# Kernel tuning notes

Hardware: AMD Instinct MI355X
Metric: run time of the kernel (lower is better)

## Reference

```python
import jax, jax.numpy as jnp
import numpy as np

TEMP = 0.5  # init kwarg `tmp`
NUM_CLASSES = 100


def setup_inputs() -> dict:
    key = jax.random.key(0)
    k1, k2 = jax.random.split(key)
    embedding = jax.random.normal(k1, (8192, 256), dtype=jnp.float32)
    label = jax.random.randint(k2, (8192,), 0, NUM_CLASSES, dtype=jnp.int64)
    return {"embedding": embedding, "label": label}


def reference(embedding, label):
    # Row-normalize -> pairwise cosine similarity [N, N]
    normed = embedding / jnp.linalg.norm(embedding, axis=1, keepdims=True)
    sim = (normed @ normed.T) / TEMP  # already divided by temperature

    N = embedding.shape[0]
    eye = jnp.eye(N, dtype=bool)

    # Denominator: sum of exp(sim) over off-diagonal entries per row
    exp_sim = jnp.exp(sim)
    row_sum = jnp.sum(jnp.where(eye, 0.0, exp_sim), axis=1)  # [N]

    # log(exp(sim_ij) / row_sum_i) = sim_ij - log(row_sum_i)
    log_prob = sim - jnp.log(row_sum)[:, None]

    # Positive mask: same label, i != j
    pos_mask = (label[:, None] == label[None, :]) & ~eye
    n_i = jnp.sum(pos_mask, axis=1)  # positives per anchor

    inner = jnp.sum(jnp.where(pos_mask, log_prob, 0.0), axis=1)  # [N]
    per_anchor = jnp.where(n_i > 0, -inner / jnp.maximum(n_i, 1).astype(sim.dtype), 0.0)
    return jnp.sum(per_anchor)
```

## Files before the change

kernel.cpp:

```cpp
#include <hip/hip_runtime.h>
#include <hip/hip_bf16.h>
#include <stdint.h>

#define N    8192
#define D    256
#define NCLS 100

static constexpr float TEMP    = 0.5f;
static constexpr float SCALE_F = 1.69864360f;
static constexpr float LN2     = 0.69314718055994531f;

typedef float f32x4 __attribute__((ext_vector_type(4)));

__device__ __forceinline__ unsigned short f2bf(float f) {
  union { float f; unsigned int u; } x; x.f = f;
  unsigned int r = x.u + 0x7fffu + ((x.u >> 16) & 1u);
  return (unsigned short)(r >> 16);
}
__device__ __forceinline__ float bf2f(unsigned short b) {
  union { unsigned int u; float f; } x; x.u = ((unsigned int)b) << 16;
  return x.f;
}


__global__ __launch_bounds__(256) void normalize_kernel(
    const float* __restrict__ emb, const long long* __restrict__ label,
    unsigned short* __restrict__ abf, unsigned char* __restrict__ a8,
    float* __restrict__ rowsum, int* __restrict__ cnt,
    int* __restrict__ list) {
  const int row  = blockIdx.x * 4 + (threadIdx.x >> 6);
  const int lane = threadIdx.x & 63;
  const float4 v = ((const float4*)(emb + (size_t)row * D))[lane];
  float ss = v.x * v.x + v.y * v.y + v.z * v.z + v.w * v.w;
#pragma unroll
  for (int off = 1; off < 64; off <<= 1) ss += __shfl_xor(ss, off);
  const float s = rsqrtf(ss) * SCALE_F;
  const float x = v.x * s, y = v.y * s, z = v.z * s, wv = v.w * s;

  ushort4 o;
  o.x = f2bf(x); o.y = f2bf(y); o.z = f2bf(z); o.w = f2bf(wv);
  ((ushort4*)(abf + (size_t)row * D))[lane] = o;

  int p = __builtin_amdgcn_cvt_pk_fp8_f32(x, y, 0, false);
  p = __builtin_amdgcn_cvt_pk_fp8_f32(z, wv, p, true);
  *(int*)(a8 + (size_t)(row >> 4) * 4096 + (lane >> 1) * 128 +
          (row & 15) * 8 + (lane & 1) * 4) = p;

  if (lane == 0) {
    rowsum[row] = 0.f;
    const int c = (int)label[row];
    const int slot = atomicAdd(cnt + c, 1);
    list[c * 256 + slot] = row;
  }
}

__global__ __launch_bounds__(256, 4) void simexp_rowsum_kernel(
    const unsigned char* __restrict__ A, float* __restrict__ rowsum) {
  const int tid  = threadIdx.x;
  const int w    = tid >> 6;
  const int lane = tid & 63;
  const int quad = lane >> 4;
  const int l15  = lane & 15;

  const int b = blockIdx.x;
  int x = (int)((-1.0f + sqrtf(1.0f + 8.0f * (float)b)) * 0.5f);
  while ((x + 1) * (x + 2) / 2 <= b) ++x;
  while (x * (x + 1) / 2 > b) --x;
  const int y = b - x * (x + 1) / 2;

  const int row0 = y << 7;
  const int col0 = x << 7;
  const bool diag = (x == y);
  const int wm  = (w & 1) * 64;
  const int jn0 = (w >> 1) * 64;
  if (diag && wm > jn0) return;
  const bool needmask = diag && (wm == jn0);

  const unsigned char* Ap = A + (size_t)((row0 >> 4) + (w & 1) * 4) * 4096;
  const unsigned char* Bp = A + (size_t)((col0 >> 4) + (w >> 1) * 4) * 4096;

  f32x4 acc[4][4];
#pragma unroll
  for (int mt = 0; mt < 4; ++mt)
#pragma unroll
    for (int nt = 0; nt < 4; ++nt) acc[mt][nt] = (f32x4){0.f, 0.f, 0.f, 0.f};

#pragma unroll
  for (int kq = 0; kq < 4; ++kq) {
#pragma unroll
    for (int kkl = 0; kkl < 2; ++kkl) {
      const int fo = kq * 1024 + (kkl * 4 + quad) * 128 + l15 * 8;
      long af[4], bf[4];
#pragma unroll
      for (int mt = 0; mt < 4; ++mt)
        af[mt] = *(const long*)(Ap + mt * 4096 + fo);
#pragma unroll
      for (int nt = 0; nt < 4; ++nt)
        bf[nt] = *(const long*)(Bp + nt * 4096 + fo);
#pragma unroll
      for (int mt = 0; mt < 4; ++mt)
#pragma unroll
        for (int nt = 0; nt < 4; ++nt)
          acc[mt][nt] = __builtin_amdgcn_mfma_f32_16x16x32_fp8_fp8(
              af[mt], bf[nt], acc[mt][nt], 0, 0, 0);
    }
  }

  float rowpart[4][4];
  float colpart[4] = {0.f, 0.f, 0.f, 0.f};
#pragma unroll
  for (int mt = 0; mt < 4; ++mt)
#pragma unroll
    for (int e = 0; e < 4; ++e) rowpart[mt][e] = 0.f;
#pragma unroll
  for (int mt = 0; mt < 4; ++mt)
#pragma unroll
    for (int nt = 0; nt < 4; ++nt)
#pragma unroll
      for (int e = 0; e < 4; ++e) {
        float v = __builtin_amdgcn_exp2f(acc[mt][nt][e]);
        if (needmask) {
          const int iw = mt * 16 + quad * 4 + e;
          const int jw = nt * 16 + l15;
          v = (iw < jw) ? v : 0.f;
        }
        rowpart[mt][e] += v;
        colpart[nt] += v;
      }

#pragma unroll
  for (int nt = 0; nt < 4; ++nt) {
    float v = colpart[nt];
    v += __shfl_xor(v, 16);
    v += __shfl_xor(v, 32);
    if (quad == 0)
      atomicAdd(&rowsum[col0 + jn0 + nt * 16 + l15], v);
  }
#pragma unroll
  for (int mt = 0; mt < 4; ++mt)
#pragma unroll
    for (int e = 0; e < 4; ++e) {
      float v = rowpart[mt][e];
      v += __shfl_xor(v, 1);
      v += __shfl_xor(v, 2);
      v += __shfl_xor(v, 4);
      v += __shfl_xor(v, 8);
      if (l15 == 0)
        atomicAdd(&rowsum[row0 + wm + mt * 16 + quad * 4 + e], v);
    }
}

__global__ __launch_bounds__(256) void finalize_kernel(
    const unsigned short* __restrict__ abf, const float* __restrict__ rowsum,
    const long long* __restrict__ label, const int* __restrict__ cnt,
    const int* __restrict__ list, float* __restrict__ out) {
  __shared__ float red[4];
  __shared__ int rows_l[256];
  const int tid  = threadIdx.x;
  const int w    = tid >> 6;
  const int lane = tid & 63;

  if (blockIdx.x < NCLS) {
    const int c = blockIdx.x;
    const int m = cnt[c];
    if (m <= 1) return;
    if (tid < m) rows_l[tid] = list[c * 256 + tid];
    __syncthreads();
    float acc = 0.f;
    for (int s = 0; s < m; ++s)
      acc += bf2f(abf[(size_t)rows_l[s] * D + tid]);
    float v = acc * acc;
#pragma unroll
    for (int off = 1; off < 64; off <<= 1) v += __shfl_xor(v, off);
    if (lane == 0) red[w] = v;
    __syncthreads();
    if (tid == 0) {
      const float ssq = red[0] + red[1] + red[2] + red[3];
      const float term = (ssq * LN2 - 2.0f * (float)m) / (float)(m - 1);
      atomicAdd(out, -term);
    }
  } else {
    const int i = (blockIdx.x - NCLS) * 256 + tid;
    const int c = (int)label[i];
    float v = 0.f;
    if (cnt[c] > 1)
      v = __builtin_amdgcn_logf(rowsum[i]) * LN2;
#pragma unroll
    for (int off = 1; off < 64; off <<= 1) v += __shfl_xor(v, off);
    if (lane == 0) red[w] = v;
    __syncthreads();
    if (tid == 0)
      atomicAdd(out, red[0] + red[1] + red[2] + red[3]);
  }
}

extern "C" void kernel_launch(void* const* d_in, const int* in_sizes, int n_in,
                              void* d_out, int out_size, void* d_ws,
                              size_t ws_size, hipStream_t stream) {
  const float* emb = (const float*)d_in[0];
  const long long* label = (const long long*)d_in[1];
  float* out = (float*)d_out;

  char* ws = (char*)d_ws;
  unsigned short* abf = (unsigned short*)ws;
  unsigned char* a8 = (unsigned char*)(ws + (size_t)N * D * 2);
  float* rowsum = (float*)(ws + (size_t)N * D * 3);
  int* cnt = (int*)(rowsum + N);
  int* list = cnt + 128;

  hipMemsetAsync(cnt, 0, 128 * 4, stream);
  hipMemsetAsync(out, 0, sizeof(float), stream);

  normalize_kernel<<<N / 4, 256, 0, stream>>>(emb, label, abf, a8, rowsum,
                                              cnt, list);

  simexp_rowsum_kernel<<<2080, 256, 0, stream>>>(a8, rowsum);

  finalize_kernel<<<NCLS + N / 256, 256, 0, stream>>>(abf, rowsum, label, cnt,
                                                      list, out);
}
```

Measured before the change: 135.9 us.

## Replace rowsum atomics with deterministic partial-sum slots reduced in finalize

Each wave of the triangular similarity kernel now writes its row and column partial exp-sums to dedicated slots in a per-band partial buffer instead of doing global atomicAdds on rowsum. The finalize kernel sums the 130 slots for each row before taking the log. Skipped diagonal waves zero their slots so every slot is written. This removes atomic contention and the rowsum zeroing, at the cost of a larger workspace and a strided 130-element reduction per row in finalize.

```diff
diff --git a/kernel.cpp b/kernel.cpp
--- a/kernel.cpp
+++ b/kernel.cpp
@@ -9,6 +9,8 @@
 static constexpr float TEMP    = 0.5f;
 static constexpr float SCALE_F = 1.69864360f;
 static constexpr float LN2     = 0.69314718055994531f;
+
+#define NSLOT 130
 
 typedef float f32x4 __attribute__((ext_vector_type(4)));
 
@@ -26,8 +28,7 @@
 __global__ __launch_bounds__(256) void normalize_kernel(
     const float* __restrict__ emb, const long long* __restrict__ label,
     unsigned short* __restrict__ abf, unsigned char* __restrict__ a8,
-    float* __restrict__ rowsum, int* __restrict__ cnt,
-    int* __restrict__ list) {
+    int* __restrict__ cnt, int* __restrict__ list) {
   const int row  = blockIdx.x * 4 + (threadIdx.x >> 6);
   const int lane = threadIdx.x & 63;
   const float4 v = ((const float4*)(emb + (size_t)row * D))[lane];
@@ -47,7 +48,6 @@
           (row & 15) * 8 + (lane & 1) * 4) = p;
 
   if (lane == 0) {
-    rowsum[row] = 0.f;
     const int c = (int)label[row];
     const int slot = atomicAdd(cnt + c, 1);
     list[c * 256 + slot] = row;
@@ -55,7 +55,7 @@
 }
 
 __global__ __launch_bounds__(256, 4) void simexp_rowsum_kernel(
-    const unsigned char* __restrict__ A, float* __restrict__ rowsum) {
+    const unsigned char* __restrict__ A, float* __restrict__ part) {
   const int tid  = threadIdx.x;
   const int w    = tid >> 6;
   const int lane = tid & 63;
@@ -73,7 +73,12 @@
   const bool diag = (x == y);
   const int wm  = (w & 1) * 64;
   const int jn0 = (w >> 1) * 64;
-  if (diag && wm > jn0) return;
+
+  if (diag && wm > jn0) {
+    part[((size_t)y * NSLOT + 2 * x + 0) * 128 + 64 + lane] = 0.f;
+    part[((size_t)x * NSLOT + 128 + 1) * 128 + lane] = 0.f;
+    return;
+  }
   const bool needmask = diag && (wm == jn0);
 
   const unsigned char* Ap = A + (size_t)((row0 >> 4) + (w & 1) * 4) * 4096;
@@ -128,13 +133,17 @@
         colpart[nt] += v;
       }
 
+  const int rslot = 2 * x + (jn0 >> 6);
+  const int cslot = diag ? (128 + (wm >> 6)) : (2 * y + (wm >> 6));
+  float* rowdst = part + ((size_t)y * NSLOT + rslot) * 128 + wm;
+  float* coldst = part + ((size_t)x * NSLOT + cslot) * 128 + jn0;
+
 #pragma unroll
   for (int nt = 0; nt < 4; ++nt) {
     float v = colpart[nt];
     v += __shfl_xor(v, 16);
     v += __shfl_xor(v, 32);
-    if (quad == 0)
-      atomicAdd(&rowsum[col0 + jn0 + nt * 16 + l15], v);
+    if (quad == 0) coldst[nt * 16 + l15] = v;
   }
 #pragma unroll
   for (int mt = 0; mt < 4; ++mt)
@@ -145,13 +154,12 @@
       v += __shfl_xor(v, 2);
       v += __shfl_xor(v, 4);
       v += __shfl_xor(v, 8);
-      if (l15 == 0)
-        atomicAdd(&rowsum[row0 + wm + mt * 16 + quad * 4 + e], v);
+      if (l15 == 0) rowdst[mt * 16 + quad * 4 + e] = v;
     }
 }
 
 __global__ __launch_bounds__(256) void finalize_kernel(
-    const unsigned short* __restrict__ abf, const float* __restrict__ rowsum,
+    const unsigned short* __restrict__ abf, const float* __restrict__ part,
     const long long* __restrict__ label, const int* __restrict__ cnt,
     const int* __restrict__ list, float* __restrict__ out) {
   __shared__ float red[4];
@@ -181,10 +189,15 @@
     }
   } else {
     const int i = (blockIdx.x - NCLS) * 256 + tid;
+    const int band = i >> 7, r = i & 127;
+    const float* ps = part + (size_t)band * NSLOT * 128 + r;
+    float rs = 0.f;
+#pragma unroll 13
+    for (int s = 0; s < NSLOT; ++s) rs += ps[(size_t)s * 128];
     const int c = (int)label[i];
     float v = 0.f;
     if (cnt[c] > 1)
-      v = __builtin_amdgcn_logf(rowsum[i]) * LN2;
+      v = __builtin_amdgcn_logf(rs) * LN2;
 #pragma unroll
     for (int off = 1; off < 64; off <<= 1) v += __shfl_xor(v, off);
     if (lane == 0) red[w] = v;
@@ -204,18 +217,17 @@
   char* ws = (char*)d_ws;
   unsigned short* abf = (unsigned short*)ws;
   unsigned char* a8 = (unsigned char*)(ws + (size_t)N * D * 2);
-  float* rowsum = (float*)(ws + (size_t)N * D * 3);
-  int* cnt = (int*)(rowsum + N);
+  float* part = (float*)(ws + (size_t)N * D * 3);
+  int* cnt = (int*)(ws + (size_t)N * D * 3 + (size_t)64 * NSLOT * 128 * 4);
   int* list = cnt + 128;
 
   hipMemsetAsync(cnt, 0, 128 * 4, stream);
   hipMemsetAsync(out, 0, sizeof(float), stream);
 
-  normalize_kernel<<<N / 4, 256, 0, stream>>>(emb, label, abf, a8, rowsum,
-                                              cnt, list);
-
-  simexp_rowsum_kernel<<<2080, 256, 0, stream>>>(a8, rowsum);
-
-  finalize_kernel<<<NCLS + N / 256, 256, 0, stream>>>(abf, rowsum, label, cnt,
+  normalize_kernel<<<N / 4, 256, 0, stream>>>(emb, label, abf, a8, cnt, list);
+
+  simexp_rowsum_kernel<<<2080, 256, 0, stream>>>(a8, part);
+
+  finalize_kernel<<<NCLS + N / 256, 256, 0, stream>>>(abf, part, label, cnt,
                                                       list, out);
 }
```

Result: faster. 130.6 us (-3.8%).
